# Performance work log

Hardware: AMD Instinct MI355X
Metric: run time of the kernel (lower is better)

The kernel has to match this reference:

```python
import jax, jax.numpy as jnp
import numpy as np

B, S, D = 4, 2048, 1024
H, DK, DV = 16, 64, 64
SCALE = 8.0  # scaling_factor = sqrt(dk)


def setup_inputs() -> dict:
    key = jax.random.key(0)
    ks = jax.random.split(key, 9)
    s = 1.0 / np.sqrt(D)
    return {
        "q": jax.random.normal(ks[0], (B, S, D), jnp.float32),
        "k": jax.random.normal(ks[1], (B, S, D), jnp.float32),
        "v": jax.random.normal(ks[2], (B, S, D), jnp.float32),
        "Wq": jax.random.uniform(ks[3], (D, H * DK), jnp.float32, -s, s),
        "bq": jax.random.uniform(ks[4], (H * DK,), jnp.float32, -s, s),
        "Wk": jax.random.uniform(ks[5], (D, H * DK), jnp.float32, -s, s),
        "bk": jax.random.uniform(ks[6], (H * DK,), jnp.float32, -s, s),
        "Wv": jax.random.uniform(ks[7], (D, H * DV), jnp.float32, -s, s),
        "bv": jax.random.uniform(ks[8], (H * DV,), jnp.float32, -s, s),
    }


def reference(q, k, v, Wq, bq, Wk, bk, Wv, bv):
    # Linear projections, then split heads: [B,S,H*d] -> [B,S,H,d]
    qh = (q @ Wq + bq).reshape(B, S, H, DK)
    kh = (k @ Wk + bk).reshape(B, S, H, DK)
    vh = (v @ Wv + bv).reshape(B, S, H, DV)
    # scores: [B,H,Sq,Sk]
    e = jnp.einsum("bqhd,bkhd->bhqk", qh, kh) / SCALE
    attn = jax.nn.softmax(e, axis=-1)
    out = jnp.einsum("bhqk,bkhd->bqhd", attn, vh)  # [B,Sq,H,DV]
    return out.reshape(B, S, H * DV)  # dropout p=0 -> identity
```

## Files before the change

### kernel.cpp

```cpp
#include <hip/hip_runtime.h>
#include <hip/hip_bf16.h>


typedef unsigned short u16;
typedef unsigned int   u32;
typedef short bf16x8 __attribute__((ext_vector_type(8)));
typedef short bf16x4 __attribute__((ext_vector_type(4)));
typedef float f32x4  __attribute__((ext_vector_type(4)));
typedef u32   u32x4  __attribute__((ext_vector_type(4)));

#define S_TOT 2048
#define HD    1024
#define QK_SCALE 0.18033688f

#if __has_builtin(__builtin_amdgcn_exp2f)
#define EXP2(x) __builtin_amdgcn_exp2f(x)
#else
#define EXP2(x) exp2f(x)
#endif

__device__ __forceinline__ u16 f2bf(float f) {
  union { float f; unsigned u; } v; v.f = f;
  unsigned r = v.u + 0x7FFFu + ((v.u >> 16) & 1u);
  return (u16)(r >> 16);
}

__device__ __forceinline__ u32 cvt_pk_bf16(float lo, float hi) {
  u32 r;
  asm("v_cvt_pk_bf16_f32 %0, %1, %2" : "=v"(r) : "v"(lo), "v"(hi));
  return r;
}

__device__ __forceinline__ bf16x4 ds_tr16(unsigned a) {
  bf16x4 d;
  asm volatile("ds_read_b64_tr_b16 %0, %1" : "=v"(d) : "v"(a) : "memory");
  return d;
}

#define LGKM_FENCE() do { asm volatile("s_waitcnt lgkmcnt(0)" ::: "memory"); \
                          __builtin_amdgcn_sched_barrier(0); } while (0)

__global__ __launch_bounds__(256)
void conv_kernel(const float* __restrict__ w0, const float* __restrict__ w1, const float* __restrict__ w2,
                 u16* __restrict__ Wt)
{
  const int z = blockIdx.y;
  const int t = threadIdx.x;
  const float* W = z == 0 ? w0 : (z == 1 ? w1 : w2);
  u16* Wz = Wt + (size_t)z * 1048576;
  int tid = blockIdx.x * 256 + t;
#pragma unroll
  for (int i = 0; i < 8; ++i) {
    int c = tid + i * 32768;
    int n = c & 1023, k4 = (c >> 10) * 4;
    float wv0 = W[(size_t)(k4 + 0) * 1024 + n];
    float wv1 = W[(size_t)(k4 + 1) * 1024 + n];
    float wv2 = W[(size_t)(k4 + 2) * 1024 + n];
    float wv3 = W[(size_t)(k4 + 3) * 1024 + n];
    int kl = k4 & 31;
    int kp = 8 * ((kl & 15) >> 2) + 4 * ((kl >> 4) & 1);
    int off = ((n >> 7) * 32 + (k4 >> 5)) * 4096 + (n & 127) * 32 + kp;
    bf16x4 sv = { (short)f2bf(wv0), (short)f2bf(wv1), (short)f2bf(wv2), (short)f2bf(wv3) };
    *(bf16x4*)&Wz[off] = sv;
  }
}

__global__ __launch_bounds__(256)
void gemm_kernel(const float* __restrict__ x0, const float* __restrict__ x1, const float* __restrict__ x2,
                 const u16* __restrict__ Wt,
                 const float* __restrict__ b0, const float* __restrict__ b1, const float* __restrict__ b2,
                 u16* __restrict__ o0, u16* __restrict__ o1, u16* __restrict__ vT)
{
  int p  = blockIdx.x + 8 * blockIdx.y + 512 * blockIdx.z;
  int wk = (p & 7) * 192 + (p >> 3);
  int nb = wk & 7, mb = (wk >> 3) & 63, z = wk >> 9;

  const float* X  = z == 0 ? x0 : (z == 1 ? x1 : x2);
  const u16*   Wz = Wt + (size_t)z * 1048576;
  const float* BS = z == 0 ? b0 : (z == 1 ? b1 : b2);
  const float  osc = (z == 0) ? QK_SCALE : 1.0f;

  const int t = threadIdx.x;
  const int lane = t & 63, wid = t >> 6;
  const int g = lane >> 4, ln = lane & 15;
  const int mbase = mb * 128, nbase = nb * 128;
  const int xr = (ln & 6) << 2;

  __shared__ __align__(16) u16 Al[128 * 32];

  f32x4 acc[4][4];
#pragma unroll
  for (int i = 0; i < 4; ++i)
#pragma unroll
    for (int j = 0; j < 4; ++j) { acc[i][j][0]=0.f; acc[i][j][1]=0.f; acc[i][j][2]=0.f; acc[i][j][3]=0.f; }

  const int arow = t >> 3;
  const int ak0  = (t & 7) * 4;
  const int ap   = 8 * ((ak0 & 15) >> 2) + 4 * ((ak0 >> 4) & 1);
  const int axr  = (arow & 6) << 2;
  const int apw  = ap ^ axr;
  const float* xp = &X[(size_t)(mbase + arow) * 1024 + ak0];

  const int whalf = wid & 1;
  const u16* wfp = Wz + (size_t)(nb * 32) * 4096 + (whalf * 64 + ln) * 32 + g * 8;
  auto loadB = [&](int kb, bf16x8* dst) __attribute__((always_inline)) {
#pragma unroll
    for (int nf = 0; nf < 4; ++nf)
      dst[nf] = *(const bf16x8*)(wfp + (size_t)kb * 4096 + nf * 512);
  };

  float4 xrg[4];
  bf16x8 bA[4], bB[4];

#pragma unroll
  for (int ps = 0; ps < 4; ++ps)
    xrg[ps] = *(const float4*)(xp + (size_t)(32 * ps) * 1024);
  xp += 32;
  loadB(0, bA);

  const int wm = wid >> 1;

  auto phase = [&](int kb, const bf16x8* bq, bf16x8* bnext, bool swapped)
      __attribute__((always_inline)) {
#pragma unroll
    for (int ps = 0; ps < 4; ++ps) {
      int row = arow + 32 * ps;
      bf16x4 sv = { (short)f2bf(xrg[ps].x), (short)f2bf(xrg[ps].y),
                    (short)f2bf(xrg[ps].z), (short)f2bf(xrg[ps].w) };
      *(bf16x4*)&Al[row * 32 + apw] = sv;
    }
    __syncthreads();

    if (kb < 31) {
#pragma unroll
      for (int ps = 0; ps < 4; ++ps)
        xrg[ps] = *(const float4*)(xp + (size_t)(32 * ps) * 1024);
      xp += 32;
      loadB(kb + 1, bnext);
    }

    bf16x8 af[4];
#pragma unroll
    for (int mf = 0; mf < 4; ++mf)
      af[mf] = *(const bf16x8*)&Al[(wm * 64 + mf * 16 + ln) * 32 + (g * 8 ^ xr)];
    __builtin_amdgcn_s_setprio(1);
    if (!swapped) {
#pragma unroll
      for (int mf = 0; mf < 4; ++mf)
#pragma unroll
        for (int nf = 0; nf < 4; ++nf)
          acc[mf][nf] = __builtin_amdgcn_mfma_f32_16x16x32_bf16(af[mf], bq[nf], acc[mf][nf], 0, 0, 0);
    } else {
#pragma unroll
      for (int mf = 0; mf < 4; ++mf)
#pragma unroll
        for (int nf = 0; nf < 4; ++nf)
          acc[mf][nf] = __builtin_amdgcn_mfma_f32_16x16x32_bf16(bq[mf], af[nf], acc[mf][nf], 0, 0, 0);
    }
    __builtin_amdgcn_s_setprio(0);
    __syncthreads();
  };

  const bool swapped = (z == 2);
  for (int it = 0; it < 16; ++it) {
    phase(2 * it,     bA, bB, swapped);
    phase(2 * it + 1, bB, bA, swapped);
  }

  if (!swapped) {
    u16* O = z == 0 ? o0 : o1;
#pragma unroll
    for (int nf = 0; nf < 4; ++nf) {
      int n = nbase + whalf * 64 + nf * 16 + ln;
      float bv = BS[n];
#pragma unroll
      for (int mf = 0; mf < 4; ++mf)
#pragma unroll
        for (int r = 0; r < 4; ++r) {
          int m = mbase + wm * 64 + mf * 16 + 4 * g + r;
          O[(size_t)m * 1024 + n] = f2bf((acc[mf][nf][r] + bv) * osc);
        }
    }
  } else {
#pragma unroll
    for (int mf = 0; mf < 4; ++mf)
#pragma unroll
      for (int r = 0; r < 4; ++r) {
        int dvg = nbase + whalf * 64 + mf * 16 + 4 * g + r;
        float bv = BS[dvg];
        int hh = dvg >> 6, dvl = dvg & 63;
#pragma unroll
        for (int nf = 0; nf < 4; ++nf) {
          int m = mbase + wm * 64 + nf * 16 + ln;
          int bb = m >> 11, ss = m & 2047;
          vT[((size_t)(bb * 16 + hh) * 64 + dvl) * 2048 + ss] = f2bf(acc[mf][nf][r] + bv);
        }
      }
  }
}

__global__ __launch_bounds__(256)
void proj_kernel(const float* __restrict__ x0, const float* __restrict__ x1, const float* __restrict__ x2,
                 const float* __restrict__ w0, const float* __restrict__ w1, const float* __restrict__ w2,
                 const float* __restrict__ b0, const float* __restrict__ b1, const float* __restrict__ b2,
                 u16* __restrict__ o0, u16* __restrict__ o1, u16* __restrict__ vT)
{
  int p  = blockIdx.x + 8 * blockIdx.y + 512 * blockIdx.z;
  int wk = (p & 7) * 192 + (p >> 3);
  int nb = wk & 7, mb = (wk >> 3) & 63, z = wk >> 9;

  const float* X  = z == 0 ? x0 : (z == 1 ? x1 : x2);
  const float* W  = z == 0 ? w0 : (z == 1 ? w1 : w2);
  const float* BS = z == 0 ? b0 : (z == 1 ? b1 : b2);
  const float  osc = (z == 0) ? QK_SCALE : 1.0f;

  const int t = threadIdx.x;
  const int lane = t & 63, wid = t >> 6;
  const int g = lane >> 4, ln = lane & 15;
  const int wm = wid >> 1, wn = wid & 1;
  const int mbase = mb * 128, nbase = nb * 128;

  __shared__ __align__(16) u16 As[128 * 40];
  __shared__ __align__(16) u16 Bs[16 * 272];

  f32x4 acc[4][4];
#pragma unroll
  for (int i = 0; i < 4; ++i)
#pragma unroll
    for (int j = 0; j < 4; ++j) { acc[i][j][0]=0.f; acc[i][j][1]=0.f; acc[i][j][2]=0.f; acc[i][j][3]=0.f; }

  const int arow = t >> 3;
  const int ak0  = (t & 7) * 4;
  const int ap   = 8 * ((ak0 & 15) >> 2) + 4 * (ak0 >> 4);
  const int bkr  = t >> 5;
  const int bnc  = (t & 31) * 4;
  const int bnblk = bnc >> 4, bncl = bnc & 15;

  const unsigned bs_base = (unsigned)(size_t)&Bs[0];

  for (int kb = 0; kb < 32; ++kb) {
    const int kbase = kb * 32;
#pragma unroll
    for (int ps = 0; ps < 4; ++ps) {
      int row = arow + 32 * ps;
      const float4 xv = *(const float4*)&X[(size_t)(mbase + row) * 1024 + kbase + ak0];
      bf16x4 sv = { (short)f2bf(xv.x), (short)f2bf(xv.y), (short)f2bf(xv.z), (short)f2bf(xv.w) };
      *(bf16x4*)&As[row * 40 + ap] = sv;
    }
#pragma unroll
    for (int ps = 0; ps < 4; ++ps) {
      int kr = bkr + 8 * ps;
      const float4 wv = *(const float4*)&W[(size_t)(kbase + kr) * 1024 + nbase + bnc];
      bf16x4 sv = { (short)f2bf(wv.x), (short)f2bf(wv.y), (short)f2bf(wv.z), (short)f2bf(wv.w) };
      *(bf16x4*)&Bs[(bnblk * 2 + (kr >> 4)) * 272 + (kr & 15) * 16 + bncl] = sv;
    }
    __syncthreads();

    bf16x8 af[4];
#pragma unroll
    for (int mf = 0; mf < 4; ++mf)
      af[mf] = *(const bf16x8*)&As[(wm * 64 + mf * 16 + ln) * 40 + g * 8];

    bf16x8 bfv[4];
#pragma unroll
    for (int nf = 0; nf < 4; ++nf) {
      unsigned base = bs_base + (unsigned)(((wn * 4 + nf) * 2) * 544) + lane * 8;
      bf16x4 lo = ds_tr16(base);
      bf16x4 hi = ds_tr16(base + 544);
      bf16x8 bb;
      bb[0]=lo[0]; bb[1]=lo[1]; bb[2]=lo[2]; bb[3]=lo[3];
      bb[4]=hi[0]; bb[5]=hi[1]; bb[6]=hi[2]; bb[7]=hi[3];
      bfv[nf] = bb;
    }
    LGKM_FENCE();
#pragma unroll
    for (int mf = 0; mf < 4; ++mf)
#pragma unroll
      for (int nf = 0; nf < 4; ++nf)
        acc[mf][nf] = __builtin_amdgcn_mfma_f32_16x16x32_bf16(af[mf], bfv[nf], acc[mf][nf], 0, 0, 0);
    __syncthreads();
  }

#pragma unroll
  for (int nf = 0; nf < 4; ++nf) {
    int n = nbase + wn * 64 + nf * 16 + ln;
    float bv = BS[n];
#pragma unroll
    for (int mf = 0; mf < 4; ++mf)
#pragma unroll
      for (int r = 0; r < 4; ++r) {
        int m = mbase + wm * 64 + mf * 16 + 4 * g + r;
        float val = (acc[mf][nf][r] + bv) * osc;
        if (z < 2) {
          u16* O = z == 0 ? o0 : o1;
          O[(size_t)m * 1024 + n] = f2bf(val);
        } else {
          vT[((size_t)((m >> 11) * 16 + (n >> 6)) * 64 + (n & 63)) * 2048 + (m & 2047)] = f2bf(val);
        }
      }
  }
}

__global__ __launch_bounds__(512)
void attn_kernel(const u16* __restrict__ qh, const u16* __restrict__ kh, const u16* __restrict__ vT,
                 float* __restrict__ out)
{
  int p  = blockIdx.x + 8 * blockIdx.y + 128 * blockIdx.z;
  int wk = (p & 7) * 64 + (p >> 3);
  int qt = wk & 7, h = (wk >> 3) & 15, b = wk >> 7;

  const int t = threadIdx.x;
  const int lane = t & 63, wid = t >> 6;
  const int g = lane >> 4, ln = lane & 15;
  const size_t bS = (size_t)b * S_TOT;
  const int qwin = qt * 256 + wid * 32;

  __shared__ __align__(16) u16 Ks[64 * 72];
  __shared__ __align__(16) u16 Vt[64 * 72];

  bf16x8 qf[2][2];
#pragma unroll
  for (int nf = 0; nf < 2; ++nf) {
    const u16* qrow = &qh[(bS + qwin + nf * 16 + ln) * HD + h * 64];
#pragma unroll
    for (int kk = 0; kk < 2; ++kk) {
      bf16x4 lo = *(const bf16x4*)&qrow[kk * 32 + 4 * g];
      bf16x4 hi = *(const bf16x4*)&qrow[kk * 32 + 4 * g + 16];
      bf16x8 qq;
      qq[0]=lo[0]; qq[1]=lo[1]; qq[2]=lo[2]; qq[3]=lo[3];
      qq[4]=hi[0]; qq[5]=hi[1]; qq[6]=hi[2]; qq[7]=hi[3];
      qf[nf][kk] = qq;
    }
  }

  bf16x8 ones;
#pragma unroll
  for (int j = 0; j < 8; ++j) ones[j] = (short)0x3F80;

  f32x4 o[2][4];
#pragma unroll
  for (int i = 0; i < 2; ++i)
#pragma unroll
    for (int j = 0; j < 4; ++j) { o[i][j][0]=0.f; o[i][j][1]=0.f; o[i][j][2]=0.f; o[i][j][3]=0.f; }
  f32x4 o1[2];
  o1[0][0]=0.f; o1[0][1]=0.f; o1[0][2]=0.f; o1[0][3]=0.f;
  o1[1][0]=0.f; o1[1][1]=0.f; o1[1][2]=0.f; o1[1][3]=0.f;

  const int skv = t >> 4;
  const int sd0 = (t & 15) * 4;
  const int kpos = 32 * (sd0 >> 5) + 8 * ((sd0 & 15) >> 2) + 4 * ((sd0 >> 4) & 1);
  u16* ksw[2];
  ksw[0] = &Ks[skv * 72 + kpos];
  ksw[1] = &Ks[(skv + 32) * 72 + kpos];
  const u16* kp = &kh[(bS + skv) * HD + h * 64 + sd0];

  const int vdv  = t >> 3;
  const int vkv8 = (t & 7) * 8;
  const int vp0  = 32 * (vkv8 >> 5) + 8 * ((vkv8 & 15) >> 2) + 4 * ((vkv8 >> 4) & 1);
  const int vkv4 = vkv8 + 4;
  const int vp1  = 32 * (vkv4 >> 5) + 8 * ((vkv4 & 15) >> 2) + 4 * ((vkv4 >> 4) & 1);
  u16* vsw0 = &Vt[vdv * 72 + vp0];
  u16* vsw1 = &Vt[vdv * 72 + vp1];
  const u16* vp = &vT[((size_t)(b * 16 + h) * 64 + vdv) * 2048 + vkv8];

  const size_t KSTEP = (size_t)64 * HD, C32 = (size_t)32 * HD;

  bf16x4 kr[2];
  kr[0] = *(const bf16x4*)kp; kr[1] = *(const bf16x4*)(kp + C32);
  bf16x8 vr = *(const bf16x8*)vp;
  kp += KSTEP; vp += 64;

  for (int it = 0; it < 32; ++it) {
    *(bf16x4*)ksw[0] = kr[0];
    *(bf16x4*)ksw[1] = kr[1];
    bf16x4 vlo = { vr[0], vr[1], vr[2], vr[3] };
    bf16x4 vhi = { vr[4], vr[5], vr[6], vr[7] };
    *(bf16x4*)vsw0 = vlo;
    *(bf16x4*)vsw1 = vhi;
    __syncthreads();

    if (it < 31) {
      kr[0] = *(const bf16x4*)kp; kr[1] = *(const bf16x4*)(kp + C32);
      vr = *(const bf16x8*)vp;
      kp += KSTEP; vp += 64;
    }

#pragma unroll
    for (int s = 0; s < 2; ++s) {
      bf16x8 kf[2][2];
#pragma unroll
      for (int mf = 0; mf < 2; ++mf)
#pragma unroll
        for (int kk = 0; kk < 2; ++kk)
          kf[mf][kk] = *(const bf16x8*)&Ks[(s * 32 + mf * 16 + ln) * 72 + kk * 32 + 8 * g];

      f32x4 sc[2][2];
      __builtin_amdgcn_s_setprio(1);
#pragma unroll
      for (int mf = 0; mf < 2; ++mf)
#pragma unroll
        for (int nf = 0; nf < 2; ++nf) {
          f32x4 a; a[0]=0.f; a[1]=0.f; a[2]=0.f; a[3]=0.f;
#pragma unroll
          for (int kk = 0; kk < 2; ++kk)
            a = __builtin_amdgcn_mfma_f32_16x16x32_bf16(kf[mf][kk], qf[nf][kk], a, 0, 0, 0);
          sc[mf][nf] = a;
        }
      __builtin_amdgcn_s_setprio(0);

      bf16x8 vf[4];
#pragma unroll
      for (int nf = 0; nf < 4; ++nf)
        vf[nf] = *(const bf16x8*)&Vt[(nf * 16 + ln) * 72 + s * 32 + 8 * g];

      bf16x8 pa[2];
#pragma unroll
      for (int nf = 0; nf < 2; ++nf) {
        float pv[2][4];
#pragma unroll
        for (int mf = 0; mf < 2; ++mf)
#pragma unroll
          for (int r = 0; r < 4; ++r)
            pv[mf][r] = EXP2(sc[mf][nf][r]);
        union { u32x4 u; bf16x8 b; } pk;
        pk.u[0] = cvt_pk_bf16(pv[0][0], pv[0][1]);
        pk.u[1] = cvt_pk_bf16(pv[0][2], pv[0][3]);
        pk.u[2] = cvt_pk_bf16(pv[1][0], pv[1][1]);
        pk.u[3] = cvt_pk_bf16(pv[1][2], pv[1][3]);
        pa[nf] = pk.b;
      }

      __builtin_amdgcn_s_setprio(1);
#pragma unroll
      for (int mq = 0; mq < 2; ++mq) {
#pragma unroll
        for (int nf = 0; nf < 4; ++nf)
          o[mq][nf] = __builtin_amdgcn_mfma_f32_16x16x32_bf16(pa[mq], vf[nf], o[mq][nf], 0, 0, 0);
        o1[mq] = __builtin_amdgcn_mfma_f32_16x16x32_bf16(pa[mq], ones, o1[mq], 0, 0, 0);
      }
      __builtin_amdgcn_s_setprio(0);
    }
    __syncthreads();
  }

#pragma unroll
  for (int mq = 0; mq < 2; ++mq)
#pragma unroll
    for (int r = 0; r < 4; ++r) {
      float inv = 1.0f / o1[mq][r];
      int qrow = qwin + mq * 16 + 4 * g + r;
#pragma unroll
      for (int nf = 0; nf < 4; ++nf)
        out[(bS + qrow) * HD + h * 64 + nf * 16 + ln] = o[mq][nf][r] * inv;
    }
}

extern "C" void kernel_launch(void* const* d_in, const int* in_sizes, int n_in,
                              void* d_out, int out_size, void* d_ws, size_t ws_size,
                              hipStream_t stream) {
  const float* q  = (const float*)d_in[0];
  const float* k  = (const float*)d_in[1];
  const float* v  = (const float*)d_in[2];
  const float* Wq = (const float*)d_in[3];
  const float* bq = (const float*)d_in[4];
  const float* Wk = (const float*)d_in[5];
  const float* bk = (const float*)d_in[6];
  const float* Wv = (const float*)d_in[7];
  const float* bv = (const float*)d_in[8];
  float* out = (float*)d_out;

  u16* qh = (u16*)d_ws;
  u16* kh = qh + (size_t)8192 * 1024;
  u16* vT = kh + (size_t)8192 * 1024;

  const size_t XB_OFF = (size_t)3 * 8192 * 1024;
  const size_t WT_OFF = XB_OFF + (size_t)3 * 8192 * 1024;
  const size_t NEED   = (WT_OFF + (size_t)3 * 1024 * 1024) * 2;

  if (ws_size >= NEED) {
    u16* Wt = (u16*)d_ws + WT_OFF;
    conv_kernel<<<dim3(128, 3), 256, 0, stream>>>(Wq, Wk, Wv, Wt);
    gemm_kernel<<<dim3(8, 64, 3), 256, 0, stream>>>(q, k, v, Wt, bq, bk, bv, qh, kh, vT);
  } else {
    proj_kernel<<<dim3(8, 64, 3), 256, 0, stream>>>(q, k, v, Wq, Wk, Wv, bq, bk, bv, qh, kh, vT);
  }
  attn_kernel<<<dim3(8, 16, 4), 512, 0, stream>>>(qh, kh, vT, out);
}
```

Before: 152.9 us.

## Double K-tile depth per barrier in projection GEMM and attention loops

The projection GEMM now stages a 64-wide K slab of activations in shared memory per iteration, with a new XOR swizzle, and prefetches two weight fragments ahead. This halves the number of barrier pairs per K sweep. The attention kernel likewise loads 128 keys/values per iteration instead of 64, halving its barrier count. The cost is more shared memory and more registers per block, which may reduce occupancy.

```diff
diff --git a/kernel.cpp b/kernel.cpp
--- a/kernel.cpp
+++ b/kernel.cpp
@@ -84,9 +84,8 @@
   const int lane = t & 63, wid = t >> 6;
   const int g = lane >> 4, ln = lane & 15;
   const int mbase = mb * 128, nbase = nb * 128;
-  const int xr = (ln & 6) << 2;
-
-  __shared__ __align__(16) u16 Al[128 * 32];
+
+  __shared__ __align__(16) u16 Al[128 * 64];
 
   f32x4 acc[4][4];
 #pragma unroll
@@ -97,11 +96,12 @@
   const int arow = t >> 3;
   const int ak0  = (t & 7) * 4;
   const int ap   = 8 * ((ak0 & 15) >> 2) + 4 * ((ak0 >> 4) & 1);
-  const int axr  = (arow & 6) << 2;
-  const int apw  = ap ^ axr;
+  const int axr  = (arow & 7) << 3;
+  const int xro  = (ln & 7) << 3;
   const float* xp = &X[(size_t)(mbase + arow) * 1024 + ak0];
 
   const int whalf = wid & 1;
+  const int wm = wid >> 1;
   const u16* wfp = Wz + (size_t)(nb * 32) * 4096 + (whalf * 64 + ln) * 32 + g * 8;
   auto loadB = [&](int kb, bf16x8* dst) __attribute__((always_inline)) {
 #pragma unroll
@@ -109,40 +109,36 @@
       dst[nf] = *(const bf16x8*)(wfp + (size_t)kb * 4096 + nf * 512);
   };
 
-  float4 xrg[4];
-  bf16x8 bA[4], bB[4];
-
-#pragma unroll
-  for (int ps = 0; ps < 4; ++ps)
-    xrg[ps] = *(const float4*)(xp + (size_t)(32 * ps) * 1024);
-  xp += 32;
-  loadB(0, bA);
-
-  const int wm = wid >> 1;
-
-  auto phase = [&](int kb, const bf16x8* bq, bf16x8* bnext, bool swapped)
-      __attribute__((always_inline)) {
-#pragma unroll
-    for (int ps = 0; ps < 4; ++ps) {
-      int row = arow + 32 * ps;
-      bf16x4 sv = { (short)f2bf(xrg[ps].x), (short)f2bf(xrg[ps].y),
-                    (short)f2bf(xrg[ps].z), (short)f2bf(xrg[ps].w) };
-      *(bf16x4*)&Al[row * 32 + apw] = sv;
-    }
-    __syncthreads();
-
-    if (kb < 31) {
+  float4 xrg[2][4];
+  bf16x8 bq0[4], bq1[4];
+
+  auto loadX = [&]() __attribute__((always_inline)) {
+#pragma unroll
+    for (int kt = 0; kt < 2; ++kt)
 #pragma unroll
       for (int ps = 0; ps < 4; ++ps)
-        xrg[ps] = *(const float4*)(xp + (size_t)(32 * ps) * 1024);
-      xp += 32;
-      loadB(kb + 1, bnext);
-    }
-
+        xrg[kt][ps] = *(const float4*)(xp + (size_t)(32 * ps) * 1024 + kt * 32);
+    xp += 64;
+  };
+  auto writeA = [&]() __attribute__((always_inline)) {
+#pragma unroll
+    for (int kt = 0; kt < 2; ++kt) {
+      int col = ((kt * 32 + ap) ^ axr);
+#pragma unroll
+      for (int ps = 0; ps < 4; ++ps) {
+        bf16x4 sv = { (short)f2bf(xrg[kt][ps].x), (short)f2bf(xrg[kt][ps].y),
+                      (short)f2bf(xrg[kt][ps].z), (short)f2bf(xrg[kt][ps].w) };
+        *(bf16x4*)&Al[(arow + 32 * ps) * 64 + col] = sv;
+      }
+    }
+  };
+
+  const bool swapped = (z == 2);
+  auto computeT = [&](int kt, const bf16x8* bq) __attribute__((always_inline)) {
     bf16x8 af[4];
 #pragma unroll
     for (int mf = 0; mf < 4; ++mf)
-      af[mf] = *(const bf16x8*)&Al[(wm * 64 + mf * 16 + ln) * 32 + (g * 8 ^ xr)];
+      af[mf] = *(const bf16x8*)&Al[(wm * 64 + mf * 16 + ln) * 64 + ((kt * 32 + g * 8) ^ xro)];
     __builtin_amdgcn_s_setprio(1);
     if (!swapped) {
 #pragma unroll
@@ -158,13 +154,21 @@
           acc[mf][nf] = __builtin_amdgcn_mfma_f32_16x16x32_bf16(bq[mf], af[nf], acc[mf][nf], 0, 0, 0);
     }
     __builtin_amdgcn_s_setprio(0);
-    __syncthreads();
   };
 
-  const bool swapped = (z == 2);
+  loadX();
+  loadB(0, bq0);
+  loadB(1, bq1);
+
   for (int it = 0; it < 16; ++it) {
-    phase(2 * it,     bA, bB, swapped);
-    phase(2 * it + 1, bB, bA, swapped);
+    writeA();
+    __syncthreads();
+    if (it < 15) loadX();
+    computeT(0, bq0);
+    if (it < 15) loadB(2 * it + 2, bq0);
+    computeT(1, bq1);
+    if (it < 15) loadB(2 * it + 3, bq1);
+    __syncthreads();
   }
 
   if (!swapped) {
@@ -315,8 +319,8 @@
   const size_t bS = (size_t)b * S_TOT;
   const int qwin = qt * 256 + wid * 32;
 
-  __shared__ __align__(16) u16 Ks[64 * 72];
-  __shared__ __align__(16) u16 Vt[64 * 72];
+  __shared__ __align__(16) u16 Ks[128 * 72];
+  __shared__ __align__(16) u16 Vt[64 * 136];
 
   bf16x8 qf[2][2];
 #pragma unroll
@@ -349,44 +353,49 @@
   const int skv = t >> 4;
   const int sd0 = (t & 15) * 4;
   const int kpos = 32 * (sd0 >> 5) + 8 * ((sd0 & 15) >> 2) + 4 * ((sd0 >> 4) & 1);
-  u16* ksw[2];
-  ksw[0] = &Ks[skv * 72 + kpos];
-  ksw[1] = &Ks[(skv + 32) * 72 + kpos];
+  u16* ksw[4];
+#pragma unroll
+  for (int c = 0; c < 4; ++c) ksw[c] = &Ks[(skv + 32 * c) * 72 + kpos];
   const u16* kp = &kh[(bS + skv) * HD + h * 64 + sd0];
 
-  const int vdv  = t >> 3;
-  const int vkv8 = (t & 7) * 8;
-  const int vp0  = 32 * (vkv8 >> 5) + 8 * ((vkv8 & 15) >> 2) + 4 * ((vkv8 >> 4) & 1);
-  const int vkv4 = vkv8 + 4;
-  const int vp1  = 32 * (vkv4 >> 5) + 8 * ((vkv4 & 15) >> 2) + 4 * ((vkv4 >> 4) & 1);
-  u16* vsw0 = &Vt[vdv * 72 + vp0];
-  u16* vsw1 = &Vt[vdv * 72 + vp1];
-  const u16* vp = &vT[((size_t)(b * 16 + h) * 64 + vdv) * 2048 + vkv8];
-
-  const size_t KSTEP = (size_t)64 * HD, C32 = (size_t)32 * HD;
-
-  bf16x4 kr[2];
-  kr[0] = *(const bf16x4*)kp; kr[1] = *(const bf16x4*)(kp + C32);
-  bf16x8 vr = *(const bf16x8*)vp;
-  kp += KSTEP; vp += 64;
-
-  for (int it = 0; it < 32; ++it) {
-    *(bf16x4*)ksw[0] = kr[0];
-    *(bf16x4*)ksw[1] = kr[1];
-    bf16x4 vlo = { vr[0], vr[1], vr[2], vr[3] };
-    bf16x4 vhi = { vr[4], vr[5], vr[6], vr[7] };
-    *(bf16x4*)vsw0 = vlo;
-    *(bf16x4*)vsw1 = vhi;
-    __syncthreads();
-
-    if (it < 31) {
-      kr[0] = *(const bf16x4*)kp; kr[1] = *(const bf16x4*)(kp + C32);
-      vr = *(const bf16x8*)vp;
-      kp += KSTEP; vp += 64;
-    }
-
-#pragma unroll
-    for (int s = 0; s < 2; ++s) {
+  const int vdv   = t >> 3;
+  const int vkv16 = (t & 7) * 16;
+  const int vc32  = vkv16 >> 5, vhi = (vkv16 >> 4) & 1;
+  u16* vsw[4];
+#pragma unroll
+  for (int j = 0; j < 4; ++j) vsw[j] = &Vt[vdv * 136 + vc32 * 32 + 8 * j + 4 * vhi];
+  const u16* vp = &vT[((size_t)(b * 16 + h) * 64 + vdv) * 2048 + vkv16];
+
+  const size_t KSTEP = (size_t)128 * HD, C32 = (size_t)32 * HD;
+
+  bf16x4 kr[4]; bf16x8 vra, vrb;
+#pragma unroll
+  for (int c = 0; c < 4; ++c) kr[c] = *(const bf16x4*)(kp + c * C32);
+  vra = *(const bf16x8*)vp; vrb = *(const bf16x8*)(vp + 8);
+  kp += KSTEP; vp += 128;
+
+  for (int it = 0; it < 16; ++it) {
+#pragma unroll
+    for (int c = 0; c < 4; ++c) *(bf16x4*)ksw[c] = kr[c];
+    {
+      bf16x4 w0 = { vra[0], vra[1], vra[2], vra[3] };
+      bf16x4 w1 = { vra[4], vra[5], vra[6], vra[7] };
+      bf16x4 w2 = { vrb[0], vrb[1], vrb[2], vrb[3] };
+      bf16x4 w3 = { vrb[4], vrb[5], vrb[6], vrb[7] };
+      *(bf16x4*)vsw[0] = w0; *(bf16x4*)vsw[1] = w1;
+      *(bf16x4*)vsw[2] = w2; *(bf16x4*)vsw[3] = w3;
+    }
+    __syncthreads();
+
+    if (it < 15) {
+#pragma unroll
+      for (int c = 0; c < 4; ++c) kr[c] = *(const bf16x4*)(kp + c * C32);
+      vra = *(const bf16x8*)vp; vrb = *(const bf16x8*)(vp + 8);
+      kp += KSTEP; vp += 128;
+    }
+
+#pragma unroll
+    for (int s = 0; s < 4; ++s) {
       bf16x8 kf[2][2];
 #pragma unroll
       for (int mf = 0; mf < 2; ++mf)
@@ -411,7 +420,7 @@
       bf16x8 vf[4];
 #pragma unroll
       for (int nf = 0; nf < 4; ++nf)
-        vf[nf] = *(const bf16x8*)&Vt[(nf * 16 + ln) * 72 + s * 32 + 8 * g];
+        vf[nf] = *(const bf16x8*)&Vt[(nf * 16 + ln) * 136 + s * 32 + 8 * g];
 
       bf16x8 pa[2];
 #pragma unroll
```

New measurement: 153.7 us. Within noise of the previous version (+0.6%).

## Double K-tile depth in projection GEMM to halve barriers per iteration

Applied to the files above, without the earlier changes.

The projection GEMM now stages a 64-wide K slab of activations in shared memory per iteration instead of 32, processing two MFMA sub-tiles between barrier pairs. This halves the number of __syncthreads per K loop and restructures the prefetch of X and weight fragments to interleave with the two compute sub-steps. The XOR swizzle is widened to match the 64-column row. It costs double the LDS for the A tile and more registers for the prefetched activations, which may reduce occupancy.

```diff
diff --git a/kernel.cpp b/kernel.cpp
--- a/kernel.cpp
+++ b/kernel.cpp
@@ -84,9 +84,8 @@
   const int lane = t & 63, wid = t >> 6;
   const int g = lane >> 4, ln = lane & 15;
   const int mbase = mb * 128, nbase = nb * 128;
-  const int xr = (ln & 6) << 2;
-
-  __shared__ __align__(16) u16 Al[128 * 32];
+
+  __shared__ __align__(16) u16 Al[128 * 64];
 
   f32x4 acc[4][4];
 #pragma unroll
@@ -97,11 +96,12 @@
   const int arow = t >> 3;
   const int ak0  = (t & 7) * 4;
   const int ap   = 8 * ((ak0 & 15) >> 2) + 4 * ((ak0 >> 4) & 1);
-  const int axr  = (arow & 6) << 2;
-  const int apw  = ap ^ axr;
+  const int axr  = (arow & 7) << 3;
+  const int xro  = (ln & 7) << 3;
   const float* xp = &X[(size_t)(mbase + arow) * 1024 + ak0];
 
   const int whalf = wid & 1;
+  const int wm = wid >> 1;
   const u16* wfp = Wz + (size_t)(nb * 32) * 4096 + (whalf * 64 + ln) * 32 + g * 8;
   auto loadB = [&](int kb, bf16x8* dst) __attribute__((always_inline)) {
 #pragma unroll
@@ -109,40 +109,36 @@
       dst[nf] = *(const bf16x8*)(wfp + (size_t)kb * 4096 + nf * 512);
   };
 
-  float4 xrg[4];
-  bf16x8 bA[4], bB[4];
-
-#pragma unroll
-  for (int ps = 0; ps < 4; ++ps)
-    xrg[ps] = *(const float4*)(xp + (size_t)(32 * ps) * 1024);
-  xp += 32;
-  loadB(0, bA);
-
-  const int wm = wid >> 1;
-
-  auto phase = [&](int kb, const bf16x8* bq, bf16x8* bnext, bool swapped)
-      __attribute__((always_inline)) {
-#pragma unroll
-    for (int ps = 0; ps < 4; ++ps) {
-      int row = arow + 32 * ps;
-      bf16x4 sv = { (short)f2bf(xrg[ps].x), (short)f2bf(xrg[ps].y),
-                    (short)f2bf(xrg[ps].z), (short)f2bf(xrg[ps].w) };
-      *(bf16x4*)&Al[row * 32 + apw] = sv;
-    }
-    __syncthreads();
-
-    if (kb < 31) {
+  float4 xrg[2][4];
+  bf16x8 bq0[4], bq1[4];
+
+  auto loadX = [&]() __attribute__((always_inline)) {
+#pragma unroll
+    for (int kt = 0; kt < 2; ++kt)
 #pragma unroll
       for (int ps = 0; ps < 4; ++ps)
-        xrg[ps] = *(const float4*)(xp + (size_t)(32 * ps) * 1024);
-      xp += 32;
-      loadB(kb + 1, bnext);
-    }
-
+        xrg[kt][ps] = *(const float4*)(xp + (size_t)(32 * ps) * 1024 + kt * 32);
+    xp += 64;
+  };
+  auto writeA = [&]() __attribute__((always_inline)) {
+#pragma unroll
+    for (int kt = 0; kt < 2; ++kt) {
+      int col = ((kt * 32 + ap) ^ axr);
+#pragma unroll
+      for (int ps = 0; ps < 4; ++ps) {
+        bf16x4 sv = { (short)f2bf(xrg[kt][ps].x), (short)f2bf(xrg[kt][ps].y),
+                      (short)f2bf(xrg[kt][ps].z), (short)f2bf(xrg[kt][ps].w) };
+        *(bf16x4*)&Al[(arow + 32 * ps) * 64 + col] = sv;
+      }
+    }
+  };
+
+  const bool swapped = (z == 2);
+  auto computeT = [&](int kt, const bf16x8* bq) __attribute__((always_inline)) {
     bf16x8 af[4];
 #pragma unroll
     for (int mf = 0; mf < 4; ++mf)
-      af[mf] = *(const bf16x8*)&Al[(wm * 64 + mf * 16 + ln) * 32 + (g * 8 ^ xr)];
+      af[mf] = *(const bf16x8*)&Al[(wm * 64 + mf * 16 + ln) * 64 + ((kt * 32 + g * 8) ^ xro)];
     __builtin_amdgcn_s_setprio(1);
     if (!swapped) {
 #pragma unroll
@@ -158,13 +154,21 @@
           acc[mf][nf] = __builtin_amdgcn_mfma_f32_16x16x32_bf16(bq[mf], af[nf], acc[mf][nf], 0, 0, 0);
     }
     __builtin_amdgcn_s_setprio(0);
-    __syncthreads();
   };
 
-  const bool swapped = (z == 2);
+  loadX();
+  loadB(0, bq0);
+  loadB(1, bq1);
+
   for (int it = 0; it < 16; ++it) {
-    phase(2 * it,     bA, bB, swapped);
-    phase(2 * it + 1, bB, bA, swapped);
+    writeA();
+    __syncthreads();
+    if (it < 15) loadX();
+    computeT(0, bq0);
+    if (it < 15) loadB(2 * it + 2, bq0);
+    computeT(1, bq1);
+    if (it < 15) loadB(2 * it + 3, bq1);
+    __syncthreads();
   }
 
   if (!swapped) {
```

Result: no change. 153.1 us, median of 3 (+0.1%).
